# Kernel tuning notes

Hardware: AMD Instinct MI355X
Metric: run time of the kernel (lower is better)

Reference implementation:

```python
import jax, jax.numpy as jnp
import numpy as np

B, T, C = 8, 2048, 1024
DFF = 4 * C
EPS = 1e-5


def _ln(h, w, b):
    mu = jnp.mean(h, axis=-1, keepdims=True)
    var = jnp.mean((h - mu) ** 2, axis=-1, keepdims=True)
    return (h - mu) * jax.lax.rsqrt(var + EPS) * w + b


def setup_inputs() -> dict:
    key = jax.random.key(0)
    ks = jax.random.split(key, 8)
    s = lambda fan_in: 1.0 / np.sqrt(fan_in)
    return {
        "x": jax.random.normal(ks[0], (B, T, C), jnp.float32),
        "w_router": jax.random.normal(ks[1], (1, C), jnp.float32) * s(C),
        "ln1_w": jnp.ones((C,), jnp.float32),
        "ln1_b": jnp.zeros((C,), jnp.float32),
        "w_qkv": jax.random.normal(ks[2], (3 * C, C), jnp.float32) * s(C),
        "b_qkv": jnp.zeros((3 * C,), jnp.float32),
        "w_o": jax.random.normal(ks[3], (C, C), jnp.float32) * s(C),
        "b_o": jnp.zeros((C,), jnp.float32),
        "ln2_w": jnp.ones((C,), jnp.float32),
        "ln2_b": jnp.zeros((C,), jnp.float32),
        "w_fc": jax.random.normal(ks[4], (DFF, C), jnp.float32) * s(C),
        "b_fc": jnp.zeros((DFF,), jnp.float32),
        "w_proj": jax.random.normal(ks[5], (C, DFF), jnp.float32) * s(DFF),
        "b_proj": jnp.zeros((C,), jnp.float32),
        "top_k": 1024,
        "n_head": 16,
    }


def _gpt2_block(h, ln1_w, ln1_b, w_qkv, b_qkv, w_o, b_o, ln2_w, ln2_b,
                w_fc, b_fc, w_proj, b_proj, n_head):
    Bq, S, Cm = h.shape
    dh = Cm // n_head
    a = _ln(h, ln1_w, ln1_b)
    qkv = a @ w_qkv.T + b_qkv                         # [B,S,3C]
    q, k, v = jnp.split(qkv, 3, axis=-1)
    q = q.reshape(Bq, S, n_head, dh)
    k = k.reshape(Bq, S, n_head, dh)
    v = v.reshape(Bq, S, n_head, dh)
    scores = jnp.einsum("bqhd,bkhd->bhqk", q, k) / np.sqrt(dh)
    causal = jnp.tril(jnp.ones((S, S), bool))
    scores = jnp.where(causal, scores, jnp.finfo(scores.dtype).min)
    probs = jax.nn.softmax(scores, axis=-1)
    attn = jnp.einsum("bhqk,bkhd->bqhd", probs, v).reshape(Bq, S, Cm)
    h = h + attn @ w_o.T + b_o
    m = _ln(h, ln2_w, ln2_b)
    mlp = jax.nn.gelu(m @ w_fc.T + b_fc, approximate=False) @ w_proj.T + b_proj
    return h + mlp


def reference(x, w_router, ln1_w, ln1_b, w_qkv, b_qkv, w_o, b_o,
              ln2_w, ln2_b, w_fc, b_fc, w_proj, b_proj, top_k, n_head):
    # STEP 1: router logits + top-k tokens (sorted by position)
    logits = (x @ w_router.T)[..., 0]                  # [B,T]
    weights, idx = jax.lax.top_k(logits, top_k)        # [B,K]
    order = jnp.argsort(idx, axis=1)
    idx = jnp.take_along_axis(idx, order, axis=1)
    weights = jnp.take_along_axis(weights, order, axis=1)
    # STEP 2: gather reduced sequence and run the block
    tokens = jnp.take_along_axis(x, idx[..., None], axis=1)   # [B,K,C]
    processed = _gpt2_block(tokens, ln1_w, ln1_b, w_qkv, b_qkv, w_o, b_o,
                            ln2_w, ln2_b, w_fc, b_fc, w_proj, b_proj, n_head)
    # STEP 3: weighted scatter-add combine
    src = processed * weights[..., None]
    out = jax.vmap(lambda xb, ib, sb: xb.at[ib].add(sb))(x, idx, src)
    return out
```

## Files before the change

### kernel.cpp

```cpp
#include <hip/hip_runtime.h>
#include <hip/hip_bf16.h>

#define B_ 8
#define T_ 2048
#define C_ 1024
#define S_ 1024
#define H_ 16
#define DH_ 64
#define DFF_ 4096
#define M_ (B_*S_)

typedef __attribute__((ext_vector_type(8))) short bf16x8;
typedef __attribute__((ext_vector_type(4))) float f32x4;

__device__ __forceinline__ short f2bf(float f) {
  __hip_bfloat16 h = __float2bfloat16(f);
  return *reinterpret_cast<short*>(&h);
}
__device__ __forceinline__ float bf2f(short s) {
  __hip_bfloat16 h = *reinterpret_cast<__hip_bfloat16*>(&s);
  return __bfloat162float(h);
}

typedef const __attribute__((address_space(1))) unsigned int* gas_p;
typedef __attribute__((address_space(3))) unsigned int* las_p;
__device__ __forceinline__ void gload_lds16(const void* g, void* l) {
  __builtin_amdgcn_global_load_lds((gas_p)g, (las_p)l, 16, 0, 0);
}

__global__ __launch_bounds__(256) void k_router(const float* __restrict__ x,
    const float* __restrict__ wr, float* __restrict__ logits) {
  int tok = blockIdx.x * 4 + (threadIdx.x >> 6);
  int l = threadIdx.x & 63;
  const float* xr = x + (size_t)tok * C_;
  float s = 0.f;
  #pragma unroll
  for (int j = 0; j < C_/64; ++j) s += xr[l + 64*j] * wr[l + 64*j];
  #pragma unroll
  for (int m = 32; m; m >>= 1) s += __shfl_xor(s, m);
  if (l == 0) logits[tok] = s;
}

__global__ __launch_bounds__(256) void k_initmap(int* __restrict__ map) {
  int i = blockIdx.x*256 + threadIdx.x;
  ((int4*)map)[i] = make_int4(-1, -1, -1, -1);
}

__global__ __launch_bounds__(1024) void k_topk(const float* __restrict__ logits,
    int* __restrict__ idx, float* __restrict__ wts, int* __restrict__ map) {
  __shared__ unsigned long long key[2048];
  int b = blockIdx.x, t = threadIdx.x;
  for (int i = t; i < T_; i += 1024) {
    float v = logits[(size_t)b*T_ + i];
    unsigned u = __float_as_uint(v);
    unsigned so = u ^ ((u >> 31) ? 0xFFFFFFFFu : 0x80000000u);
    key[i] = ((unsigned long long)(~so) << 32) | (unsigned)i;
  }
  __syncthreads();
  for (int k = 2; k <= 2048; k <<= 1) {
    for (int j = k >> 1; j > 0; j >>= 1) {
      int i = ((t & ~(j-1)) << 1) | (t & (j-1));
      int ix = i | j;
      unsigned long long a = key[i], c = key[ix];
      bool up = ((i & k) == 0);
      if ((a > c) == up) { key[i] = c; key[ix] = a; }
      __syncthreads();
    }
  }
  unsigned long long a = key[t];
  __syncthreads();
  unsigned i0 = (unsigned)(a & 0xFFFFFFFFu);
  unsigned so = ~(unsigned)(a >> 32);
  unsigned bits = (so & 0x80000000u) ? (so ^ 0x80000000u) : ~so;
  key[t] = ((unsigned long long)i0 << 32) | bits;
  __syncthreads();
  for (int k = 2; k <= 1024; k <<= 1) {
    for (int j = k >> 1; j > 0; j >>= 1) {
      if (t < 512) {
        int i = ((t & ~(j-1)) << 1) | (t & (j-1));
        int ix = i | j;
        unsigned long long a2 = key[i], c2 = key[ix];
        bool up = ((i & k) == 0);
        if ((a2 > c2) == up) { key[i] = c2; key[ix] = a2; }
      }
      __syncthreads();
    }
  }
  int tok = (int)(key[t] >> 32);
  idx[(size_t)b*S_ + t] = tok;
  wts[(size_t)b*S_ + t] = __uint_as_float((unsigned)(key[t] & 0xFFFFFFFFu));
  map[(size_t)b*T_ + tok] = t;
}

__global__ __launch_bounds__(256) void k_cvt(const float* __restrict__ s,
    short* __restrict__ d, int n4) {
  int i = blockIdx.x * 256 + threadIdx.x;
  if (i >= n4) return;
  float4 v = ((const float4*)s)[i];
  short4 o;
  o.x = f2bf(v.x); o.y = f2bf(v.y); o.z = f2bf(v.z); o.w = f2bf(v.w);
  ((short4*)d)[i] = o;
}

template<bool GATHER>
__global__ __launch_bounds__(256) void k_ln(const float* __restrict__ x,
    const int* __restrict__ idx, float* __restrict__ hbuf,
    short* __restrict__ obf, const float* __restrict__ g,
    const float* __restrict__ beta) {
  __shared__ float red[8];
  int row = blockIdx.x;
  const float* src;
  if (GATHER) {
    int b = row >> 10, k = row & 1023;
    src = x + ((size_t)b*T_ + idx[b*S_ + k]) * C_;
  } else {
    src = hbuf + (size_t)row * C_;
  }
  int t = threadIdx.x;
  float4 v = *(const float4*)(src + t*4);
  float s  = v.x + v.y + v.z + v.w;
  float s2 = v.x*v.x + v.y*v.y + v.z*v.z + v.w*v.w;
  #pragma unroll
  for (int m = 32; m; m >>= 1) { s += __shfl_xor(s, m); s2 += __shfl_xor(s2, m); }
  int w = t >> 6, lane = t & 63;
  if (lane == 0) { red[w] = s; red[w+4] = s2; }
  __syncthreads();
  s  = red[0]+red[1]+red[2]+red[3];
  s2 = red[4]+red[5]+red[6]+red[7];
  float mu = s * (1.f/(float)C_);
  float var = s2 * (1.f/(float)C_) - mu*mu;
  float rs = rsqrtf(var + 1e-5f);
  int c0 = t*4;
  float4 gw = *(const float4*)(g + c0);
  float4 bw = *(const float4*)(beta + c0);
  short4 o;
  o.x = f2bf((v.x-mu)*rs*gw.x + bw.x);
  o.y = f2bf((v.y-mu)*rs*gw.y + bw.y);
  o.z = f2bf((v.z-mu)*rs*gw.z + bw.z);
  o.w = f2bf((v.w-mu)*rs*gw.w + bw.w);
  *(short4*)(obf + (size_t)row*C_ + c0) = o;
  if (GATHER) *(float4*)(hbuf + (size_t)row*C_ + c0) = v;
}

#define EPI_BF16 0
#define EPI_GELU 1
#define EPI_ADD32 2

__device__ __forceinline__ float gelu_fast(float v) {
  float z = 0.7978845608f * (v + 0.044715f * v * v * v);
  float e = __expf(2.f * z);
  return v - v * __builtin_amdgcn_rcpf(e + 1.f);
}

template<int BM, int BN, int EPI>
__global__ __launch_bounds__(256, 2) void k_gemm7(
    const short* __restrict__ A, int lda,
    const short* __restrict__ Bp, int ldb,
    void* __restrict__ Cp, int ldc,
    const float* __restrict__ bias,
    int nNt, int Ktot) {
  constexpr int ACH = BM*64/8/256;
  constexpr int BCH = BN*64/8/256;
  __shared__ short As[2][BM*64];
  __shared__ short Bs[2][BN*64];
  int nwg = gridDim.x, orig = blockIdx.x;
  int q8 = nwg >> 3, r8 = nwg & 7;
  int xcd = orig & 7, loc = orig >> 3;
  int wg = (xcd < r8 ? xcd*(q8+1) : r8*(q8+1) + (xcd-r8)*q8) + loc;
  int bm = wg / nNt, bn = wg % nNt;
  const short* Ar = A + (size_t)bm*BM*lda;
  const short* Br = Bp + (size_t)bn*BN*ldb;
  constexpr int WM = BM/2, WN = BN/2, FM = WM/16, FN = WN/16;
  int t = threadIdx.x, lane = t & 63, w = t >> 6;
  int wm = w >> 1, wn = w & 1;
  int lr = lane & 15, kq = lane >> 4;

  auto stage = [&](int buf, int k0) {
    #pragma unroll
    for (int c = 0; c < ACH; ++c) {
      int ch = c*256 + t;
      int row = ch >> 3, sq = (ch & 7) ^ (row & 7);
      gload_lds16(Ar + (size_t)row*lda + (k0 + sq*8), &As[buf][ch*8]);
    }
    #pragma unroll
    for (int c = 0; c < BCH; ++c) {
      int ch = c*256 + t;
      int row = ch >> 3, sq = (ch & 7) ^ (row & 7);
      gload_lds16(Br + (size_t)row*ldb + (k0 + sq*8), &Bs[buf][ch*8]);
    }
  };

  f32x4 acc[FM][FN] = {};
  int NT = Ktot >> 6;
  stage(0, 0);
  __syncthreads();
  for (int kt = 0; kt < NT; ++kt) {
    int cur = kt & 1;
    if (kt + 1 < NT) stage(cur ^ 1, (kt + 1) << 6);
    const short* Ab = As[cur];
    const short* Bb = Bs[cur];
    bf16x8 af[2][FM], bfv[2][FN];
    #pragma unroll
    for (int ks = 0; ks < 2; ++ks) {
      #pragma unroll
      for (int i = 0; i < FM; ++i) {
        int ra = wm*WM + i*16 + lr;
        af[ks][i] = *(const bf16x8*)&Ab[ra*64 + ((((ks<<2)+kq) ^ (ra & 7)) << 3)];
      }
      #pragma unroll
      for (int j = 0; j < FN; ++j) {
        int rb = wn*WN + j*16 + lr;
        bfv[ks][j] = *(const bf16x8*)&Bb[rb*64 + ((((ks<<2)+kq) ^ (rb & 7)) << 3)];
      }
    }
    #pragma unroll
    for (int ks = 0; ks < 2; ++ks)
      #pragma unroll
      for (int i = 0; i < FM; ++i)
        #pragma unroll
        for (int j = 0; j < FN; ++j)
          acc[i][j] = __builtin_amdgcn_mfma_f32_16x16x32_bf16(bfv[ks][j], af[ks][i], acc[i][j], 0, 0, 0);
    if (kt + 1 < NT) __syncthreads();
  }
  int mrow0 = bm*BM + wm*WM + lr;
  int ncol0 = bn*BN + wn*WN + (kq << 2);
  #pragma unroll
  for (int i = 0; i < FM; ++i) {
    int row = mrow0 + i*16;
    #pragma unroll
    for (int j = 0; j < FN; ++j) {
      int col = ncol0 + j*16;
      float4 bv = bias ? *(const float4*)(bias + col) : make_float4(0.f,0.f,0.f,0.f);
      float v0 = acc[i][j][0] + bv.x, v1 = acc[i][j][1] + bv.y;
      float v2 = acc[i][j][2] + bv.z, v3 = acc[i][j][3] + bv.w;
      if (EPI == EPI_ADD32) {
        float* Co = (float*)Cp + (size_t)row*ldc + col;
        float4 old = *(float4*)Co;
        old.x += v0; old.y += v1; old.z += v2; old.w += v3;
        *(float4*)Co = old;
      } else {
        if (EPI == EPI_GELU) {
          v0 = gelu_fast(v0); v1 = gelu_fast(v1);
          v2 = gelu_fast(v2); v3 = gelu_fast(v3);
        }
        short4 o; o.x = f2bf(v0); o.y = f2bf(v1); o.z = f2bf(v2); o.w = f2bf(v3);
        *(short4*)((short*)Cp + (size_t)row*ldc + col) = o;
      }
    }
  }
}

__global__ __launch_bounds__(256) void k_vt(const short* __restrict__ qkv,
                                            short* __restrict__ vt) {
  __shared__ short tile[64][65];
  int blk = blockIdx.x;
  int s0 = (blk & 15) << 6;
  int bh = blk >> 4;
  int b = bh >> 4, h = bh & 15;
  const short* src = qkv + (size_t)b*S_*3*C_ + 2*C_ + h*DH_;
  int t = threadIdx.x;
  #pragma unroll
  for (int it = 0; it < 16; ++it) {
    int e = it*256 + t;
    int r = e >> 6, d = e & 63;
    tile[d][r] = src[(size_t)(s0 + r)*3*C_ + d];
  }
  __syncthreads();
  short* dst = vt + (size_t)bh*DH_*S_ + s0;
  #pragma unroll
  for (int it = 0; it < 16; ++it) {
    int e = it*256 + t;
    int d2 = e >> 6, c = e & 63;
    dst[(size_t)d2*S_ + c] = tile[d2][c];
  }
}

__global__ __launch_bounds__(256, 4) void k_fattn(
    const short* __restrict__ qkv, const short* __restrict__ vt,
    short* __restrict__ attnb) {
  __shared__ short Ks[2][64*64];
  __shared__ short Ps[4][32*72];
  int qt = blockIdx.x;
  int bh = blockIdx.y;
  int b = bh >> 4, h = bh & 15;
  int t = threadIdx.x, lane = t & 63, w = t >> 6;
  int lr = lane & 15, kq = lane >> 4;
  const short* Qbase = qkv + ((size_t)b*S_ + qt*128)*3*C_ + h*DH_;
  const short* Kbase = qkv + (size_t)b*S_*3*C_ + C_ + h*DH_;
  const short* Vtb   = vt + (size_t)bh*DH_*S_;

  short* Qs = &Ks[0][0];
  #pragma unroll
  for (int c = 0; c < 4; ++c) {
    int ch = c*256 + t;
    int row = ch >> 3, sq = (ch & 7) ^ (row & 7);
    gload_lds16(Qbase + (size_t)row*3*C_ + sq*8, &Qs[ch*8]);
  }
  asm volatile("s_waitcnt vmcnt(0)" ::: "memory");
  __builtin_amdgcn_s_barrier();
  bf16x8 qf[2][2];
  #pragma unroll
  for (int ks = 0; ks < 2; ++ks)
    #pragma unroll
    for (int i = 0; i < 2; ++i) {
      int rq = w*32 + i*16 + lr;
      qf[ks][i] = *(const bf16x8*)&Qs[rq*64 + ((((ks<<2)+kq) ^ (rq & 7)) << 3)];
    }
  asm volatile("s_waitcnt lgkmcnt(0)" ::: "memory");
  __builtin_amdgcn_sched_barrier(0);
  __builtin_amdgcn_s_barrier();

  auto stageK = [&](int buf, int jj) {
    #pragma unroll
    for (int c = 0; c < 2; ++c) {
      int ch = c*256 + t;
      int row = ch >> 3, sq = (ch & 7) ^ (row & 7);
      gload_lds16(Kbase + (size_t)(jj*64 + row)*3*C_ + sq*8, &Ks[buf][ch*8]);
    }
  };
  stageK(0, 0);

  f32x4 o[2][4] = {};
  float m_i[2] = {-3.0e38f, -3.0e38f};
  float l_i[2] = {0.f, 0.f};
  short* Pw = &Ps[w][0];
  int NTl = 2*qt + 2;

  for (int jj = 0; jj < NTl; ++jj) {
    int cur = jj & 1;
    asm volatile("s_waitcnt vmcnt(0)" ::: "memory");
    __builtin_amdgcn_s_barrier();
    if (jj + 1 < NTl) stageK(cur ^ 1, jj + 1);

    f32x4 s[2][4] = {};
    #pragma unroll
    for (int ks = 0; ks < 2; ++ks) {
      bf16x8 kf[4];
      #pragma unroll
      for (int j = 0; j < 4; ++j) {
        int rk = j*16 + lr;
        kf[j] = *(const bf16x8*)&Ks[cur][rk*64 + ((((ks<<2)+kq) ^ (rk & 7)) << 3)];
      }
      #pragma unroll
      for (int i = 0; i < 2; ++i)
        #pragma unroll
        for (int j = 0; j < 4; ++j)
          s[i][j] = __builtin_amdgcn_mfma_f32_16x16x32_bf16(kf[j], qf[ks][i], s[i][j], 0, 0, 0);
    }

    bool maskTile = (jj >= 2*qt);
    #pragma unroll
    for (int i = 0; i < 2; ++i) {
      int qrow = qt*128 + w*32 + i*16 + lr;
      float rmax = -3.0e38f;
      #pragma unroll
      for (int j = 0; j < 4; ++j)
        #pragma unroll
        for (int r = 0; r < 4; ++r) {
          int colg = jj*64 + j*16 + (kq<<2) + r;
          float v = s[i][j][r] * 0.125f;
          if (maskTile && colg > qrow) v = -3.0e38f;
          s[i][j][r] = v;
          rmax = fmaxf(rmax, v);
        }
      rmax = fmaxf(rmax, __shfl_xor(rmax, 16));
      rmax = fmaxf(rmax, __shfl_xor(rmax, 32));
      float mnew = fmaxf(m_i[i], rmax);
      float alpha = __expf(m_i[i] - mnew);
      m_i[i] = mnew;
      float rsum = 0.f;
      #pragma unroll
      for (int j = 0; j < 4; ++j)
        #pragma unroll
        for (int r = 0; r < 4; ++r) {
          float pv = __expf(s[i][j][r] - mnew);
          s[i][j][r] = pv;
          rsum += pv;
        }
      rsum += __shfl_xor(rsum, 16);
      rsum += __shfl_xor(rsum, 32);
      l_i[i] = l_i[i]*alpha + rsum;
      #pragma unroll
      for (int jo = 0; jo < 4; ++jo)
        #pragma unroll
        for (int r = 0; r < 4; ++r)
          o[i][jo][r] *= alpha;
    }

    #pragma unroll
    for (int i = 0; i < 2; ++i)
      #pragma unroll
      for (int j = 0; j < 4; ++j) {
        short4 pk;
        pk.x = f2bf(s[i][j][0]); pk.y = f2bf(s[i][j][1]);
        pk.z = f2bf(s[i][j][2]); pk.w = f2bf(s[i][j][3]);
        *(short4*)&Pw[(i*16 + lr)*72 + j*16 + (kq<<2)] = pk;
      }
    asm volatile("s_waitcnt lgkmcnt(0)" ::: "memory");
    __builtin_amdgcn_sched_barrier(0);

    #pragma unroll
    for (int sstep = 0; sstep < 2; ++sstep) {
      bf16x8 pf[2], vf[4];
      #pragma unroll
      for (int i = 0; i < 2; ++i)
        pf[i] = *(const bf16x8*)&Pw[(i*16 + lr)*72 + sstep*32 + (kq<<3)];
      #pragma unroll
      for (int jo = 0; jo < 4; ++jo)
        vf[jo] = *(const bf16x8*)&Vtb[(size_t)(jo*16 + lr)*S_ + jj*64 + sstep*32 + (kq<<3)];
      #pragma unroll
      for (int i = 0; i < 2; ++i)
        #pragma unroll
        for (int jo = 0; jo < 4; ++jo)
          o[i][jo] = __builtin_amdgcn_mfma_f32_16x16x32_bf16(vf[jo], pf[i], o[i][jo], 0, 0, 0);
    }
  }

  #pragma unroll
  for (int i = 0; i < 2; ++i) {
    float inv = 1.f / l_i[i];
    int q = qt*128 + w*32 + i*16 + lr;
    #pragma unroll
    for (int jo = 0; jo < 4; ++jo) {
      int d = jo*16 + (kq<<2);
      short4 ov;
      ov.x = f2bf(o[i][jo][0]*inv); ov.y = f2bf(o[i][jo][1]*inv);
      ov.z = f2bf(o[i][jo][2]*inv); ov.w = f2bf(o[i][jo][3]*inv);
      *(short4*)&attnb[((size_t)b*S_ + q)*C_ + h*DH_ + d] = ov;
    }
  }
}

__global__ __launch_bounds__(256) void k_combine(const float* __restrict__ x,
    const int* __restrict__ map, const float* __restrict__ wts,
    const float* __restrict__ hbuf, float* __restrict__ out) {
  int row = blockIdx.x;
  int b = row >> 11;
  int m = map[row];
  size_t o = (size_t)row*C_ + threadIdx.x*4;
  float4 xv = *(const float4*)(x + o);
  if (m >= 0) {
    float wv = wts[(size_t)b*S_ + m];
    const float* hr = hbuf + ((size_t)b*S_ + m)*C_ + threadIdx.x*4;
    float4 hv = *(const float4*)hr;
    xv.x += wv*hv.x; xv.y += wv*hv.y; xv.z += wv*hv.z; xv.w += wv*hv.w;
  }
  *(float4*)(out + o) = xv;
}

extern "C" void kernel_launch(void* const* d_in, const int* in_sizes, int n_in,
                              void* d_out, int out_size, void* d_ws, size_t ws_size,
                              hipStream_t stream) {
  const float* x     = (const float*)d_in[0];
  const float* wrt   = (const float*)d_in[1];
  const float* ln1w  = (const float*)d_in[2];
  const float* ln1b  = (const float*)d_in[3];
  const float* wqkv  = (const float*)d_in[4];
  const float* bqkv  = (const float*)d_in[5];
  const float* wo    = (const float*)d_in[6];
  const float* bo    = (const float*)d_in[7];
  const float* ln2w  = (const float*)d_in[8];
  const float* ln2b  = (const float*)d_in[9];
  const float* wfc   = (const float*)d_in[10];
  const float* bfc   = (const float*)d_in[11];
  const float* wproj = (const float*)d_in[12];
  const float* bproj = (const float*)d_in[13];
  float* out = (float*)d_out;

  char* p = (char*)d_ws;
  auto alloc = [&](size_t bytes) {
    char* r = p; p += (bytes + 255) & ~(size_t)255; return r;
  };
  float* logits = (float*)alloc((size_t)B_*T_*4);
  int*   idx    = (int*)  alloc((size_t)B_*S_*4);
  float* wts    = (float*)alloc((size_t)B_*S_*4);
  int*   map    = (int*)  alloc((size_t)B_*T_*4);
  float* hbuf   = (float*)alloc((size_t)M_*C_*4);
  short* abuf   = (short*)alloc((size_t)M_*C_*2);
  short* qkvb   = (short*)alloc((size_t)M_*3*C_*2);
  short* vtb    = (short*)alloc((size_t)B_*H_*DH_*S_*2);
  short* attnb  = (short*)alloc((size_t)M_*C_*2);
  short* fcb    = (short*)alloc((size_t)M_*DFF_*2);
  short* wqkvb  = (short*)alloc((size_t)3*C_*C_*2);
  short* wob    = (short*)alloc((size_t)C_*C_*2);
  short* wfcb   = (short*)alloc((size_t)DFF_*C_*2);
  short* wprojb = (short*)alloc((size_t)C_*DFF_*2);
  if (ws_size < (size_t)(p - (char*)d_ws)) return;

  k_cvt<<<dim3(3*C_*C_/4/256), dim3(256), 0, stream>>>(wqkv, wqkvb, 3*C_*C_/4);
  k_cvt<<<dim3(C_*C_/4/256),   dim3(256), 0, stream>>>(wo, wob, C_*C_/4);
  k_cvt<<<dim3(DFF_*C_/4/256), dim3(256), 0, stream>>>(wfc, wfcb, DFF_*C_/4);
  k_cvt<<<dim3(C_*DFF_/4/256), dim3(256), 0, stream>>>(wproj, wprojb, C_*DFF_/4);

  k_router<<<dim3(B_*T_/4), dim3(256), 0, stream>>>(x, wrt, logits);
  k_initmap<<<dim3(B_*T_/4/256), dim3(256), 0, stream>>>(map);
  k_topk<<<dim3(B_), dim3(1024), 0, stream>>>(logits, idx, wts, map);

  k_ln<true><<<dim3(M_), dim3(256), 0, stream>>>(x, idx, hbuf, abuf, ln1w, ln1b);

  k_gemm7<128,128,EPI_BF16><<<dim3((M_/128)*(3*C_/128)), dim3(256), 0, stream>>>(
      abuf, C_, wqkvb, C_, qkvb, 3*C_, bqkv, 3*C_/128, C_);

  k_vt<<<dim3(B_*H_*(S_/64)), dim3(256), 0, stream>>>(qkvb, vtb);

  k_fattn<<<dim3(S_/128, B_*H_), dim3(256), 0, stream>>>(qkvb, vtb, attnb);

  k_gemm7<128,128,EPI_ADD32><<<dim3((M_/128)*(C_/128)), dim3(256), 0, stream>>>(
      attnb, C_, wob, C_, hbuf, C_, bo, C_/128, C_);

  k_ln<false><<<dim3(M_), dim3(256), 0, stream>>>(nullptr, nullptr, hbuf, abuf, ln2w, ln2b);

  k_gemm7<128,128,EPI_GELU><<<dim3((M_/128)*(DFF_/128)), dim3(256), 0, stream>>>(
      abuf, C_, wfcb, C_, fcb, DFF_, bfc, DFF_/128, C_);

  k_gemm7<128,128,EPI_ADD32><<<dim3((M_/128)*(C_/128)), dim3(256), 0, stream>>>(
      fcb, DFF_, wprojb, DFF_, hbuf, C_, bproj, C_/128, DFF_);

  k_combine<<<dim3(B_*T_), dim3(256), 0, stream>>>(x, map, wts, hbuf, out);
}
```

Measured before the change: 493.8 us.

## Enlarge GEMM tiles to 256-row blocks with 8 waves and MFMA priority

Replaces the 128x128, 4-wave GEMM with a 256xBN tile (BN 256 or 128) run by 512 threads in 8 waves, which raises reuse of each staged operand and cuts global/LDS traffic per FLOP. The k-substep loop now interleaves LDS fragment loads with MFMAs instead of preloading both substeps, and it raises wave priority around the MFMA block with s_setprio. The LDS footprint rises to 128 KB for BN=256, which may limit occupancy (the launch bounds still ask for 2 blocks per CU). The grid also shrinks, and for the N=1024 GEMMs that can leave CUs with less work to balance.

```diff
diff --git a/kernel.cpp b/kernel.cpp
--- a/kernel.cpp
+++ b/kernel.cpp
@@ -152,15 +152,19 @@
   return v - v * __builtin_amdgcn_rcpf(e + 1.f);
 }
 
-template<int BM, int BN, int EPI>
-__global__ __launch_bounds__(256, 2) void k_gemm7(
+template<int BN, int EPI>
+__global__ __launch_bounds__(512, 2) void k_gemm8(
     const short* __restrict__ A, int lda,
     const short* __restrict__ Bp, int ldb,
     void* __restrict__ Cp, int ldc,
     const float* __restrict__ bias,
     int nNt, int Ktot) {
-  constexpr int ACH = BM*64/8/256;
-  constexpr int BCH = BN*64/8/256;
+  constexpr int BM = 256;
+  constexpr int WM_CNT = (BN == 256) ? 2 : 4;
+  constexpr int WN_CNT = 8 / WM_CNT;
+  constexpr int WM = BM / WM_CNT, WN = BN / WN_CNT;
+  constexpr int FM = WM / 16, FN = WN / 16;
+  constexpr int BCH = BN / 64;
   __shared__ short As[2][BM*64];
   __shared__ short Bs[2][BN*64];
   int nwg = gridDim.x, orig = blockIdx.x;
@@ -170,21 +174,21 @@
   int bm = wg / nNt, bn = wg % nNt;
   const short* Ar = A + (size_t)bm*BM*lda;
   const short* Br = Bp + (size_t)bn*BN*ldb;
-  constexpr int WM = BM/2, WN = BN/2, FM = WM/16, FN = WN/16;
   int t = threadIdx.x, lane = t & 63, w = t >> 6;
-  int wm = w >> 1, wn = w & 1;
+  int wm = w / WN_CNT, wn = w % WN_CNT;
   int lr = lane & 15, kq = lane >> 4;
 
-  auto stage = [&](int buf, int k0) {
-    #pragma unroll
-    for (int c = 0; c < ACH; ++c) {
-      int ch = c*256 + t;
+  auto stage = [&](int buf, int kt) {
+    int k0 = kt << 6;
+    #pragma unroll
+    for (int c = 0; c < 4; ++c) {
+      int ch = c*512 + t;
       int row = ch >> 3, sq = (ch & 7) ^ (row & 7);
       gload_lds16(Ar + (size_t)row*lda + (k0 + sq*8), &As[buf][ch*8]);
     }
     #pragma unroll
     for (int c = 0; c < BCH; ++c) {
-      int ch = c*256 + t;
+      int ch = c*512 + t;
       int row = ch >> 3, sq = (ch & 7) ^ (row & 7);
       gload_lds16(Br + (size_t)row*ldb + (k0 + sq*8), &Bs[buf][ch*8]);
     }
@@ -196,30 +200,30 @@
   __syncthreads();
   for (int kt = 0; kt < NT; ++kt) {
     int cur = kt & 1;
-    if (kt + 1 < NT) stage(cur ^ 1, (kt + 1) << 6);
+    if (kt + 1 < NT) stage(cur ^ 1, kt + 1);
     const short* Ab = As[cur];
     const short* Bb = Bs[cur];
-    bf16x8 af[2][FM], bfv[2][FN];
     #pragma unroll
     for (int ks = 0; ks < 2; ++ks) {
+      bf16x8 af[FM], bfv[FN];
+      #pragma unroll
+      for (int j = 0; j < FN; ++j) {
+        int rb = wn*WN + j*16 + lr;
+        bfv[j] = *(const bf16x8*)&Bb[rb*64 + ((((ks<<2)+kq) ^ (rb & 7)) << 3)];
+      }
       #pragma unroll
       for (int i = 0; i < FM; ++i) {
         int ra = wm*WM + i*16 + lr;
-        af[ks][i] = *(const bf16x8*)&Ab[ra*64 + ((((ks<<2)+kq) ^ (ra & 7)) << 3)];
+        af[i] = *(const bf16x8*)&Ab[ra*64 + ((((ks<<2)+kq) ^ (ra & 7)) << 3)];
       }
-      #pragma unroll
-      for (int j = 0; j < FN; ++j) {
-        int rb = wn*WN + j*16 + lr;
-        bfv[ks][j] = *(const bf16x8*)&Bb[rb*64 + ((((ks<<2)+kq) ^ (rb & 7)) << 3)];
-      }
-    }
-    #pragma unroll
-    for (int ks = 0; ks < 2; ++ks)
+      __builtin_amdgcn_s_setprio(1);
       #pragma unroll
       for (int i = 0; i < FM; ++i)
         #pragma unroll
         for (int j = 0; j < FN; ++j)
-          acc[i][j] = __builtin_amdgcn_mfma_f32_16x16x32_bf16(bfv[ks][j], af[ks][i], acc[i][j], 0, 0, 0);
+          acc[i][j] = __builtin_amdgcn_mfma_f32_16x16x32_bf16(bfv[j], af[i], acc[i][j], 0, 0, 0);
+      __builtin_amdgcn_s_setprio(0);
+    }
     if (kt + 1 < NT) __syncthreads();
   }
   int mrow0 = bm*BM + wm*WM + lr;
@@ -498,22 +502,22 @@
 
   k_ln<true><<<dim3(M_), dim3(256), 0, stream>>>(x, idx, hbuf, abuf, ln1w, ln1b);
 
-  k_gemm7<128,128,EPI_BF16><<<dim3((M_/128)*(3*C_/128)), dim3(256), 0, stream>>>(
-      abuf, C_, wqkvb, C_, qkvb, 3*C_, bqkv, 3*C_/128, C_);
+  k_gemm8<256,EPI_BF16><<<dim3((M_/256)*(3*C_/256)), dim3(512), 0, stream>>>(
+      abuf, C_, wqkvb, C_, qkvb, 3*C_, bqkv, 3*C_/256, C_);
 
   k_vt<<<dim3(B_*H_*(S_/64)), dim3(256), 0, stream>>>(qkvb, vtb);
 
   k_fattn<<<dim3(S_/128, B_*H_), dim3(256), 0, stream>>>(qkvb, vtb, attnb);
 
-  k_gemm7<128,128,EPI_ADD32><<<dim3((M_/128)*(C_/128)), dim3(256), 0, stream>>>(
+  k_gemm8<128,EPI_ADD32><<<dim3((M_/256)*(C_/128)), dim3(512), 0, stream>>>(
       attnb, C_, wob, C_, hbuf, C_, bo, C_/128, C_);
 
   k_ln<false><<<dim3(M_), dim3(256), 0, stream>>>(nullptr, nullptr, hbuf, abuf, ln2w, ln2b);
 
-  k_gemm7<128,128,EPI_GELU><<<dim3((M_/128)*(DFF_/128)), dim3(256), 0, stream>>>(
-      abuf, C_, wfcb, C_, fcb, DFF_, bfc, DFF_/128, C_);
-
-  k_gemm7<128,128,EPI_ADD32><<<dim3((M_/128)*(C_/128)), dim3(256), 0, stream>>>(
+  k_gemm8<256,EPI_GELU><<<dim3((M_/256)*(DFF_/256)), dim3(512), 0, stream>>>(
+      abuf, C_, wfcb, C_, fcb, DFF_, bfc, DFF_/256, C_);
+
+  k_gemm8<128,EPI_ADD32><<<dim3((M_/256)*(C_/128)), dim3(512), 0, stream>>>(
       fcb, DFF_, wprojb, DFF_, hbuf, C_, bproj, C_/128, DFF_);
 
   k_combine<<<dim3(B_*T_), dim3(256), 0, stream>>>(x, map, wts, hbuf, out);
```

Measured after the change: 505.9 us. 1.02x slower.

## Replace double-buffered GEMM with single-buffered BK=32 loop for occupancy

Applied to the files above, without the earlier changes.

Replaces the double-buffered 64-wide K-tile GEMM with a single-buffered 32-wide K-tile version that waits for each tile load before computing. The LDS footprint drops sharply and the second-occupancy launch bound is removed, so more workgroups can be resident and hide latency across waves instead of within one. In exchange, the kernel loses intra-block prefetch overlap, runs twice as many iterations with two barriers each, and needs a new XOR swizzle for 32-element rows.

```diff
diff --git a/kernel.cpp b/kernel.cpp
--- a/kernel.cpp
+++ b/kernel.cpp
@@ -153,16 +153,14 @@
 }
 
 template<int BM, int BN, int EPI>
-__global__ __launch_bounds__(256, 2) void k_gemm7(
+__global__ __launch_bounds__(256) void k_gemm9(
     const short* __restrict__ A, int lda,
     const short* __restrict__ Bp, int ldb,
     void* __restrict__ Cp, int ldc,
     const float* __restrict__ bias,
     int nNt, int Ktot) {
-  constexpr int ACH = BM*64/8/256;
-  constexpr int BCH = BN*64/8/256;
-  __shared__ short As[2][BM*64];
-  __shared__ short Bs[2][BN*64];
+  __shared__ short As[BM*32];
+  __shared__ short Bs[BN*32];
   int nwg = gridDim.x, orig = blockIdx.x;
   int q8 = nwg >> 3, r8 = nwg & 7;
   int xcd = orig & 7, loc = orig >> 3;
@@ -174,53 +172,39 @@
   int t = threadIdx.x, lane = t & 63, w = t >> 6;
   int wm = w >> 1, wn = w & 1;
   int lr = lane & 15, kq = lane >> 4;
-
-  auto stage = [&](int buf, int k0) {
-    #pragma unroll
-    for (int c = 0; c < ACH; ++c) {
+  f32x4 acc[FM][FN] = {};
+  for (int k0 = 0; k0 < Ktot; k0 += 32) {
+    #pragma unroll
+    for (int c = 0; c < BM/64; ++c) {
       int ch = c*256 + t;
-      int row = ch >> 3, sq = (ch & 7) ^ (row & 7);
-      gload_lds16(Ar + (size_t)row*lda + (k0 + sq*8), &As[buf][ch*8]);
-    }
-    #pragma unroll
-    for (int c = 0; c < BCH; ++c) {
+      int row = ch >> 2, sq = (ch & 3) ^ ((row ^ (row >> 2)) & 3);
+      gload_lds16(Ar + (size_t)row*lda + (k0 + sq*8), &As[ch*8]);
+    }
+    #pragma unroll
+    for (int c = 0; c < BN/64; ++c) {
       int ch = c*256 + t;
-      int row = ch >> 3, sq = (ch & 7) ^ (row & 7);
-      gload_lds16(Br + (size_t)row*ldb + (k0 + sq*8), &Bs[buf][ch*8]);
-    }
-  };
-
-  f32x4 acc[FM][FN] = {};
-  int NT = Ktot >> 6;
-  stage(0, 0);
-  __syncthreads();
-  for (int kt = 0; kt < NT; ++kt) {
-    int cur = kt & 1;
-    if (kt + 1 < NT) stage(cur ^ 1, (kt + 1) << 6);
-    const short* Ab = As[cur];
-    const short* Bb = Bs[cur];
-    bf16x8 af[2][FM], bfv[2][FN];
-    #pragma unroll
-    for (int ks = 0; ks < 2; ++ks) {
-      #pragma unroll
-      for (int i = 0; i < FM; ++i) {
-        int ra = wm*WM + i*16 + lr;
-        af[ks][i] = *(const bf16x8*)&Ab[ra*64 + ((((ks<<2)+kq) ^ (ra & 7)) << 3)];
-      }
-      #pragma unroll
-      for (int j = 0; j < FN; ++j) {
-        int rb = wn*WN + j*16 + lr;
-        bfv[ks][j] = *(const bf16x8*)&Bb[rb*64 + ((((ks<<2)+kq) ^ (rb & 7)) << 3)];
-      }
-    }
-    #pragma unroll
-    for (int ks = 0; ks < 2; ++ks)
-      #pragma unroll
-      for (int i = 0; i < FM; ++i)
-        #pragma unroll
-        for (int j = 0; j < FN; ++j)
-          acc[i][j] = __builtin_amdgcn_mfma_f32_16x16x32_bf16(bfv[ks][j], af[ks][i], acc[i][j], 0, 0, 0);
-    if (kt + 1 < NT) __syncthreads();
+      int row = ch >> 2, sq = (ch & 3) ^ ((row ^ (row >> 2)) & 3);
+      gload_lds16(Br + (size_t)row*ldb + (k0 + sq*8), &Bs[ch*8]);
+    }
+    asm volatile("s_waitcnt vmcnt(0)" ::: "memory");
+    __syncthreads();
+    bf16x8 af[FM], bfv[FN];
+    #pragma unroll
+    for (int j = 0; j < FN; ++j) {
+      int rb = wn*WN + j*16 + lr;
+      bfv[j] = *(const bf16x8*)&Bs[rb*32 + ((kq ^ ((rb ^ (rb >> 2)) & 3)) << 3)];
+    }
+    #pragma unroll
+    for (int i = 0; i < FM; ++i) {
+      int ra = wm*WM + i*16 + lr;
+      af[i] = *(const bf16x8*)&As[ra*32 + ((kq ^ ((ra ^ (ra >> 2)) & 3)) << 3)];
+    }
+    #pragma unroll
+    for (int i = 0; i < FM; ++i)
+      #pragma unroll
+      for (int j = 0; j < FN; ++j)
+        acc[i][j] = __builtin_amdgcn_mfma_f32_16x16x32_bf16(bfv[j], af[i], acc[i][j], 0, 0, 0);
+    __syncthreads();
   }
   int mrow0 = bm*BM + wm*WM + lr;
   int ncol0 = bn*BN + wn*WN + (kq << 2);
@@ -498,22 +482,22 @@
 
   k_ln<true><<<dim3(M_), dim3(256), 0, stream>>>(x, idx, hbuf, abuf, ln1w, ln1b);
 
-  k_gemm7<128,128,EPI_BF16><<<dim3((M_/128)*(3*C_/128)), dim3(256), 0, stream>>>(
+  k_gemm9<128,128,EPI_BF16><<<dim3((M_/128)*(3*C_/128)), dim3(256), 0, stream>>>(
       abuf, C_, wqkvb, C_, qkvb, 3*C_, bqkv, 3*C_/128, C_);
 
   k_vt<<<dim3(B_*H_*(S_/64)), dim3(256), 0, stream>>>(qkvb, vtb);
 
   k_fattn<<<dim3(S_/128, B_*H_), dim3(256), 0, stream>>>(qkvb, vtb, attnb);
 
-  k_gemm7<128,128,EPI_ADD32><<<dim3((M_/128)*(C_/128)), dim3(256), 0, stream>>>(
+  k_gemm9<128,128,EPI_ADD32><<<dim3((M_/128)*(C_/128)), dim3(256), 0, stream>>>(
       attnb, C_, wob, C_, hbuf, C_, bo, C_/128, C_);
 
   k_ln<false><<<dim3(M_), dim3(256), 0, stream>>>(nullptr, nullptr, hbuf, abuf, ln2w, ln2b);
 
-  k_gemm7<128,128,EPI_GELU><<<dim3((M_/128)*(DFF_/128)), dim3(256), 0, stream>>>(
+  k_gemm9<128,128,EPI_GELU><<<dim3((M_/128)*(DFF_/128)), dim3(256), 0, stream>>>(
       abuf, C_, wfcb, C_, fcb, DFF_, bfc, DFF_/128, C_);
 
-  k_gemm7<128,128,EPI_ADD32><<<dim3((M_/128)*(C_/128)), dim3(256), 0, stream>>>(
+  k_gemm9<128,128,EPI_ADD32><<<dim3((M_/128)*(C_/128)), dim3(256), 0, stream>>>(
       fcb, DFF_, wprojb, DFF_, hbuf, C_, bproj, C_/128, DFF_);
 
   k_combine<<<dim3(B_*T_), dim3(256), 0, stream>>>(x, map, wts, hbuf, out);
```

New measurement: 541.7 us. 1.1x slower.
